# Performance work log

Measured on AMD Instinct MI355X. Metric: run time of the kernel, lower is better.

## Reference

```python
import jax, jax.numpy as jnp
import numpy as np
import math

B, L, NH, HD = 2, 2048, 8, 128
C = NH * HD            # hidden size
K = 3                  # short_conv_L
EMB, ORDER = 33, 64    # hyena filter emb_dim / order


def setup_inputs() -> dict:
    key = jax.random.key(0)
    ks = jax.random.split(key, 10)
    f32 = jnp.float32
    return {
        "query_layer": jax.random.normal(ks[0], (L, B, NH, HD), f32),
        "key_layer": jax.random.normal(ks[1], (L, B, NH, HD), f32),
        "value_layer": jax.random.normal(ks[2], (L, B, NH, HD), f32),
        # depthwise short conv params: [3(qkv), C, 1, K] / [3, C]
        "short_conv_weight": jax.random.normal(ks[3], (3, C, 1, K), f32) * 0.3,
        "short_conv_bias": jax.random.normal(ks[4], (3, C), f32) * 0.02,
        # D term of the long conv, shape [head_dim]
        "long_conv_bias": jax.random.normal(ks[5], (HD,), f32) * 0.1,
        # hyena filter MLP (torch Linear convention: W [out, in])
        "lin0_w": jax.random.normal(ks[6], (ORDER, EMB), f32) * (1.0 / np.sqrt(EMB)),
        "lin0_b": jnp.zeros((ORDER,), f32),
        "lin1_w": jax.random.normal(ks[7], (ORDER, ORDER), f32) * (1.0 / np.sqrt(ORDER)),
        "lin1_b": jnp.zeros((ORDER,), f32),
        "lin2_w": jax.random.normal(ks[8], (ORDER, ORDER), f32) * (1.0 / np.sqrt(ORDER)),
        "lin2_b": jnp.zeros((ORDER,), f32),
        "freq": jnp.ones((1, ORDER), f32),  # Sin activation freq (w=1), shared across layers
        "final_w": jax.random.normal(ks[9], (HD, ORDER), f32) * (1.0 / np.sqrt(ORDER)),
        # exponential modulation decay rates, [1,1,HD], as initialized in the module
        "mod_weight": jnp.linspace(math.log(0.01) / 1.5, math.log(0.01) / 0.3, HD,
                                   dtype=f32)[None, None],
    }


def _depthwise_conv(x, w, b):
    # x [B,C,L], w [C,1,K], b [C]; causal: pad K-1 both sides, keep first L
    y = jax.lax.conv_general_dilated(
        x, w, window_strides=(1,), padding=[(K - 1, K - 1)],
        feature_group_count=C, dimension_numbers=("NCH", "OIH", "NCH"))
    return y[..., :L] + b[None, :, None]


def _hyena_filter(lin0_w, lin0_b, lin1_w, lin1_b, lin2_w, lin2_b, freq, final_w, mod_weight):
    t = jnp.linspace(0.0, 1.0, L)[None, :, None]              # [1,L,1]
    bands = (EMB - 1) // 2
    w_ang = 2.0 * jnp.pi * jnp.linspace(0.0, L - 1.0, L) / L  # [L]
    f = jnp.linspace(1e-4, bands - 1.0, bands)                # [bands]
    theta = w_ang[:, None] * f[None, :]                       # [L,bands]; z = exp(-1j f w)
    z = jnp.concatenate([t[0], jnp.cos(theta), -jnp.sin(theta)], axis=-1)[None]  # [1,L,EMB]
    h = jnp.sin(freq * (z @ lin0_w.T + lin0_b))
    h = jnp.sin(freq * (h @ lin1_w.T + lin1_b))
    h = jnp.sin(freq * (h @ lin2_w.T + lin2_b))
    h = h @ final_w.T                                         # [1,L,HD]
    h = h * jnp.exp(-t * jnp.abs(mod_weight))                 # exponential modulation
    return h[0].T                                             # [HD, L]


def _fftconv_heads(k, kern, D, q, v):
    # mirrors fftconv_heads_ref with head_dim=NH: channels split as (h=HD, d=NH)
    b = k.shape[0]
    kr = k.reshape(b, HD, NH, L).transpose(0, 2, 1, 3)  # b nh hd L  (d1 axis)
    vr = v.reshape(b, HD, NH, L).transpose(0, 2, 1, 3)  # b nh hd L  (d2 axis)
    qr = q.reshape(b, HD, NH, L).transpose(0, 2, 1, 3)  # b nh hd L
    kv = kr[:, :, None] * vr[:, None]                   # [b, nh, nh, hd, L]
    n = 2 * L
    kv_f = jnp.fft.rfft(kv, n=n) / n
    kern_f = jnp.fft.rfft(kern, n=n)                    # [HD, n//2+1]
    y = jnp.fft.irfft(kv_f * kern_f, n=n, norm="forward")[..., :L]
    out = y + kv * D[:, None]                           # D over head_dim axis
    out = (out * qr[:, :, None]).sum(axis=1)            # _mul_sum over d1 -> [b, nh, hd, L]
    return out.transpose(0, 2, 1, 3).reshape(b, C, L)   # 'b d2 h l -> b (h d2) l'


def reference(query_layer, key_layer, value_layer, short_conv_weight, short_conv_bias,
              long_conv_bias, lin0_w, lin0_b, lin1_w, lin1_b, lin2_w, lin2_b,
              freq, final_w, mod_weight):
    # 'sq b np hn -> b (np hn) sq'
    q = jnp.transpose(query_layer, (1, 2, 3, 0)).reshape(B, C, L)
    k = jnp.transpose(key_layer, (1, 2, 3, 0)).reshape(B, C, L)
    v = jnp.transpose(value_layer, (1, 2, 3, 0)).reshape(B, C, L)
    q = _depthwise_conv(q, short_conv_weight[0], short_conv_bias[0])
    k = _depthwise_conv(k, short_conv_weight[1], short_conv_bias[1])
    v = _depthwise_conv(v, short_conv_weight[2], short_conv_bias[2])
    filt = _hyena_filter(lin0_w, lin0_b, lin1_w, lin1_b, lin2_w, lin2_b,
                         freq, final_w, mod_weight)
    # module calls fftconv_heads_ref(k=value, ..., q=query, v=key)
    y = _fftconv_heads(v, filt, long_conv_bias, q=q, v=k)
    # 'b (np hn) sq -> b np sq hn'
    return y.reshape(B, NH, HD, L).transpose(0, 1, 3, 2)
```

## Files before the change

kernel.cpp:

```cpp
#include <hip/hip_runtime.h>
#include <stdint.h>
#include <string.h>

#define L_SEQ 2048
#define B_SZ 2
#define NHH 8
#define HDD 128
#define C_SZ 1024
#define EMB_D 33
#define ORD 64
#define BANDS 16
#define FSTRIDE (L_SEQ + 256)
#define FRS_S 2568
#define FRS_FILL 2176

typedef _Float16 f16;
typedef f16 f16x8 __attribute__((ext_vector_type(8)));
typedef f16 f16x4 __attribute__((ext_vector_type(4)));
typedef float f32x4 __attribute__((ext_vector_type(4)));

__global__ void filter_kernel(const float* __restrict__ w0, const float* __restrict__ b0,
                              const float* __restrict__ w1, const float* __restrict__ b1,
                              const float* __restrict__ w2, const float* __restrict__ b2,
                              const float* __restrict__ fr, const float* __restrict__ wf,
                              const float* __restrict__ md, const float* __restrict__ Dv,
                              float* __restrict__ filt) {
  int tid = threadIdx.x;
  int o = tid & 63;
  int lq = tid >> 6;
  int l = blockIdx.x * 4 + lq;

  if (blockIdx.x < 128) filt[(size_t)blockIdx.x * FSTRIDE + tid] = 0.0f;

  __shared__ float zs[4][EMB_D];
  __shared__ float hs[4][ORD];
  __shared__ float gs[4][ORD];

  float t = (float)l / (float)(L_SEQ - 1);
  float wang = 6.2831853071795864f * (float)l / (float)L_SEQ;
  const float fstep = (15.0f - 1e-4f) / 15.0f;

  if (o == 0) zs[lq][0] = t;
  if (o >= 1 && o < 1 + BANDS) {
    int j = o - 1;
    float fj = 1e-4f + fstep * (float)j;
    zs[lq][1 + j] = cosf(wang * fj);
  }
  if (o >= 1 + BANDS && o < 1 + 2 * BANDS) {
    int j = o - 1 - BANDS;
    float fj = 1e-4f + fstep * (float)j;
    zs[lq][1 + BANDS + j] = -sinf(wang * fj);
  }
  __syncthreads();

  float fo = fr[o];
  float a = b0[o];
  for (int e = 0; e < EMB_D; ++e) a += zs[lq][e] * w0[o * EMB_D + e];
  hs[lq][o] = sinf(fo * a);
  __syncthreads();

  a = b1[o];
  for (int e = 0; e < ORD; ++e) a += hs[lq][e] * w1[o * ORD + e];
  gs[lq][o] = sinf(fo * a);
  __syncthreads();

  a = b2[o];
  for (int e = 0; e < ORD; ++e) a += gs[lq][e] * w2[o * ORD + e];
  float h3 = sinf(fo * a);
  __syncthreads();
  hs[lq][o] = h3;
  __syncthreads();

  #pragma unroll
  for (int pass = 0; pass < 2; ++pass) {
    int hd = pass * 64 + o;
    float acc = 0.0f;
    for (int e = 0; e < ORD; ++e) acc += hs[lq][e] * wf[hd * ORD + e];
    float val = acc * expf(-t * fabsf(md[hd]));
    if (l == 0) val += Dv[hd];
    filt[(size_t)hd * FSTRIDE + 256 + l] = val;
  }
}

#define TLC 64
__global__ void shortconv_kernel(const float* __restrict__ q_in,
                                 const float* __restrict__ k_in,
                                 const float* __restrict__ v_in,
                                 const float* __restrict__ scw,
                                 const float* __restrict__ scb,
                                 float* __restrict__ AqT, f16* __restrict__ Akt16,
                                 f16* __restrict__ Avt16) {
  int bid = blockIdx.x;
  int lt = bid & 31;
  int np = (bid >> 5) & 7;
  int b = bid >> 8;
  int l0 = lt * TLC;
  int tid = threadIdx.x;

  __shared__ float xs[TLC + 2][HDD + 4];
  __shared__ float wcs[HDD][4];

  const float* ins[3] = {q_in, k_in, v_in};

  for (int tsr = 0; tsr < 3; ++tsr) {
    const float* x = ins[tsr];
    if (tid < HDD) {
      int c = np * HDD + tid;
      wcs[tid][0] = scw[(tsr * C_SZ + c) * 3 + 0];
      wcs[tid][1] = scw[(tsr * C_SZ + c) * 3 + 1];
      wcs[tid][2] = scw[(tsr * C_SZ + c) * 3 + 2];
      wcs[tid][3] = scb[tsr * C_SZ + c];
    }
    for (int idx = tid; idx < (TLC + 2) * HDD; idx += 256) {
      int row = idx >> 7, hn = idx & 127;
      int l = l0 - 2 + row;
      float val = 0.0f;
      if (l >= 0) val = x[(((size_t)l * B_SZ + b) * NHH + np) * HDD + hn];
      xs[row][hn] = val;
    }
    __syncthreads();

    int n1 = tid & 7;
    int lp = tid >> 3;
    for (int hdi = 0; hdi < 16; ++hdi) {
      int hn = hdi * 8 + n1;
      float cw0 = wcs[hn][0], cw1 = wcs[hn][1], cw2 = wcs[hn][2], cb = wcs[hn][3];
      int hd = np * 16 + hdi;
      #pragma unroll
      for (int half = 0; half < 2; ++half) {
        int ll = half * 32 + lp;
        float y = cb + cw0 * xs[ll][hn] + cw1 * xs[ll + 1][hn]
                     + cw2 * xs[ll + 2][hn];
        int l = l0 + ll;
        if (tsr == 0) {
          AqT[(((size_t)b * HDD + hd) * NHH + n1) * L_SEQ + l] = y;
        } else {
          int ch = l >> 7, m = l & 127;
          int off = (n1 << 8) | ((m << 1) ^ (n1 << 4));
          char* base = (tsr == 1) ? (char*)Akt16 : (char*)Avt16;
          *(f16*)(base + ((((size_t)(b * HDD + hd)) * 16 + ch) << 11) + off) = (f16)y;
        }
      }
    }
    __syncthreads();
  }
}

__global__ void __launch_bounds__(256, 3)
hyena_main(const float* __restrict__ AqT, const f16* __restrict__ Akt16,
           const f16* __restrict__ Avt16, const float* __restrict__ filt,
           float* __restrict__ out) {
  int bid = blockIdx.x;
  int pr = bid >> 8;
  int hd = bid & 127;
  int b  = (bid >> 7) & 1;
  int tid = threadIdx.x;
  int w = tid >> 6;
  int lane = tid & 63;
  int r = lane & 15;
  int p = lane >> 4;
  int a = (15 - r) & 7;

  __shared__ f16 FRS[8][FRS_S];
  __shared__ f16 AV[3][1024];
  __shared__ f16 AK[3][1024];

  const float* frow = filt + (size_t)hd * FSTRIDE + 256;
  const char* avtg = (const char*)Avt16 + (((size_t)(b * HDD + hd)) * 16 << 11);
  const char* aktg = (const char*)Akt16 + (((size_t)(b * HDD + hd)) * 16 << 11);
  const float* aqtb = AqT + ((size_t)b * HDD + hd) * NHH * L_SEQ;
  int np = hd >> 4, hnb = (hd & 15) * 8;

  for (int aa = 0; aa < 8; ++aa) {
    for (int z4 = tid * 4; z4 < FRS_FILL; z4 += 1024) {
      const float* s = frow + (2044 - aa - z4);
      float4 v;
      __builtin_memcpy(&v, s, 16);
      f16x4 o = {(f16)v.w, (f16)v.z, (f16)v.y, (f16)v.x};
      *(f16x4*)&FRS[aa][z4] = o;
    }
  }

  f32x4 acc[2][4];

  auto dma = [&](int c, int bi) {
    const char* srcb = (w >> 1) ? aktg : avtg;
    f16* dstb = (w >> 1) ? &AK[bi][(w & 1) * 512] : &AV[bi][(w & 1) * 512];
    const char* src = srcb + ((size_t)c << 11) + (w & 1) * 1024 + lane * 16;
    __builtin_amdgcn_global_load_lds((const unsigned int*)src,
                                     (unsigned int*)dstb, 16, 0, 0);
  };

  auto unit = [&](int lt, int c, int bi) {
    int dy = 2047 - (lt - c) * 128;
    int zb = dy - r - a + p * 8 - 112 + 16 * (3 - w);
    f16x8 f[6];
    #pragma unroll
    for (int j = 0; j < 6; ++j)
      f[j] = *(const f16x8*)&FRS[a][zb + 32 * j];
    int ky = r & 7;
    __builtin_amdgcn_s_setprio(1);
    #pragma unroll
    for (int s = 0; s < 4; ++s) {
      f16x8 kf = *(const f16x8*)&AK[bi][ky * 128 + ((s * 32 + p * 8) ^ (ky * 8))];
      #pragma unroll
      for (int nt = 0; nt < 4; ++nt) {
        int vy = nt * 2 + (r >> 3);
        f16x8 vf = *(const f16x8*)&AV[bi][vy * 128 + ((s * 32 + p * 8) ^ (vy * 8))];
        f16x8 bf = vf * kf;
        acc[0][nt] = __builtin_amdgcn_mfma_f32_16x16x32_f16(
            f[s + 2], bf, acc[0][nt], 0, 0, 0);
        acc[1][nt] = __builtin_amdgcn_mfma_f32_16x16x32_f16(
            f[s], bf, acc[1][nt], 0, 0, 0);
      }
    }
    __builtin_amdgcn_s_setprio(0);
  };

  auto epilogue = [&](int lt) {
    int l0 = lt * 128;
    int hi = r >> 3;
    int n2 = r & 7;
    #pragma unroll
    for (int mi = 0; mi < 2; ++mi) {
      int mt = w + 4 * mi;
      float4 qv[4];
      #pragma unroll
      for (int nt = 0; nt < 4; ++nt)
        qv[nt] = *(const float4*)(aqtb + (size_t)(nt * 2 + hi) * L_SEQ
                                  + l0 + mt * 16 + p * 4);
      #pragma unroll
      for (int reg = 0; reg < 4; ++reg) {
        float pv = qv[0][reg] * acc[mi][0][reg] + qv[1][reg] * acc[mi][1][reg]
                 + qv[2][reg] * acc[mi][2][reg] + qv[3][reg] * acc[mi][3][reg];
        pv += __shfl_xor(pv, 8, 64);
        if (r < 8) {
          int i = mt * 16 + p * 4 + reg;
          out[(((size_t)b * NHH + np) * L_SEQ + (l0 + i)) * HDD + hnb + n2] = pv;
        }
      }
    }
  };

  auto run_pass = [&](int lt, int NC) {
    #pragma unroll
    for (int mi = 0; mi < 2; ++mi)
      #pragma unroll
      for (int nt = 0; nt < 4; ++nt)
        acc[mi][nt] = f32x4{0.f, 0.f, 0.f, 0.f};
    dma(0, 0);
    if (NC > 1) dma(1, 1);
    for (int c = 0; c < NC; ++c) {
      if (c + 1 < NC)
        asm volatile("s_waitcnt vmcnt(1) lgkmcnt(0)" ::: "memory");
      else
        asm volatile("s_waitcnt vmcnt(0) lgkmcnt(0)" ::: "memory");
      __builtin_amdgcn_s_barrier();
      __builtin_amdgcn_sched_barrier(0);
      if (c + 2 < NC) {
        int bi2 = c + 2; bi2 -= (bi2 >= 3) ? 3 : 0; bi2 -= (bi2 >= 3) ? 3 : 0;
        dma(c + 2, (c + 2) % 3);
      }
      unit(lt, c, c % 3);
    }
    epilogue(lt);
    __syncthreads();
  };

  run_pass(pr, pr + 1);
  run_pass(15 - pr, 16 - pr);
}

extern "C" void kernel_launch(void* const* d_in, const int* in_sizes, int n_in,
                              void* d_out, int out_size, void* d_ws, size_t ws_size,
                              hipStream_t stream) {
  const float* q_in = (const float*)d_in[0];
  const float* k_in = (const float*)d_in[1];
  const float* v_in = (const float*)d_in[2];
  const float* scw  = (const float*)d_in[3];
  const float* scb  = (const float*)d_in[4];
  const float* Dv   = (const float*)d_in[5];
  const float* w0   = (const float*)d_in[6];
  const float* b0   = (const float*)d_in[7];
  const float* w1   = (const float*)d_in[8];
  const float* b1   = (const float*)d_in[9];
  const float* w2   = (const float*)d_in[10];
  const float* b2   = (const float*)d_in[11];
  const float* fr   = (const float*)d_in[12];
  const float* wf   = (const float*)d_in[13];
  const float* md   = (const float*)d_in[14];

  float* ws   = (float*)d_ws;
  float* filt = ws;
  float* AqT  = ws + (size_t)HDD * FSTRIDE;
  f16*   Akt16 = (f16*)(AqT + (size_t)B_SZ * HDD * L_SEQ * NHH);
  f16*   Avt16 = Akt16 + (size_t)B_SZ * HDD * 16 * 1024;

  filter_kernel<<<512, 256, 0, stream>>>(w0, b0, w1, b1, w2, b2, fr, wf, md, Dv, filt);
  shortconv_kernel<<<512, 256, 0, stream>>>(q_in, k_in, v_in, scw, scb, AqT, Akt16, Avt16);
  hyena_main<<<2048, 256, 0, stream>>>(AqT, Akt16, Avt16, filt, (float*)d_out);
}
```

Measured before the change: 148.4 us.

## Fuse the two output-tile passes to share loaded key/value chunks

The two sequential passes over output tiles (low and high) are merged into one loop over chunks. Each loaded K/V chunk and its elementwise product now feed both accumulator sets, so the low tile's chunks are not loaded twice. The pipeline moves to a 4-deep buffer processed two chunks per barrier, and the filter LDS row stride is shrunk to offset the larger buffers. The cost is doubled accumulator registers, which may reduce occupancy under the 3-blocks launch bound, and a branchy per-chunk do_lo path.

```diff
diff --git a/kernel.cpp b/kernel.cpp
--- a/kernel.cpp
+++ b/kernel.cpp
@@ -11,7 +11,7 @@
 #define ORD 64
 #define BANDS 16
 #define FSTRIDE (L_SEQ + 256)
-#define FRS_S 2568
+#define FRS_S 2184
 #define FRS_FILL 2176
 
 typedef _Float16 f16;
@@ -161,9 +161,13 @@
   int p = lane >> 4;
   int a = (15 - r) & 7;
 
+  const int LT_hi = 15 - pr;
+  const int LT_lo = pr;
+  const int NCc = 16 - pr;
+
   __shared__ f16 FRS[8][FRS_S];
-  __shared__ f16 AV[3][1024];
-  __shared__ f16 AK[3][1024];
+  __shared__ f16 AV[4][1024];
+  __shared__ f16 AK[4][1024];
 
   const float* frow = filt + (size_t)hd * FSTRIDE + 256;
   const char* avtg = (const char*)Avt16 + (((size_t)(b * HDD + hd)) * 16 << 11);
@@ -181,7 +185,14 @@
     }
   }
 
-  f32x4 acc[2][4];
+  f32x4 aH[2][4], aL[2][4];
+  #pragma unroll
+  for (int mi = 0; mi < 2; ++mi)
+    #pragma unroll
+    for (int nt = 0; nt < 4; ++nt) {
+      aH[mi][nt] = f32x4{0.f, 0.f, 0.f, 0.f};
+      aL[mi][nt] = f32x4{0.f, 0.f, 0.f, 0.f};
+    }
 
   auto dma = [&](int c, int bi) {
     const char* srcb = (w >> 1) ? aktg : avtg;
@@ -191,13 +202,21 @@
                                      (unsigned int*)dstb, 16, 0, 0);
   };
 
-  auto unit = [&](int lt, int c, int bi) {
-    int dy = 2047 - (lt - c) * 128;
-    int zb = dy - r - a + p * 8 - 112 + 16 * (3 - w);
-    f16x8 f[6];
+  auto chunk_body = [&](int c) {
+    int bi = c & 3;
+    bool do_lo = (c <= LT_lo);
+    int zcom = p * 8 - 112 + 16 * (3 - w) - r - a;
+    int zbH = 2047 - (LT_hi - c) * 128 + zcom;
+    f16x8 fH[6], fL[6];
     #pragma unroll
     for (int j = 0; j < 6; ++j)
-      f[j] = *(const f16x8*)&FRS[a][zb + 32 * j];
+      fH[j] = *(const f16x8*)&FRS[a][zbH + 32 * j];
+    if (do_lo) {
+      int zbL = 2047 - (LT_lo - c) * 128 + zcom;
+      #pragma unroll
+      for (int j = 0; j < 6; ++j)
+        fL[j] = *(const f16x8*)&FRS[a][zbL + 32 * j];
+    }
     int ky = r & 7;
     __builtin_amdgcn_s_setprio(1);
     #pragma unroll
@@ -208,16 +227,22 @@
         int vy = nt * 2 + (r >> 3);
         f16x8 vf = *(const f16x8*)&AV[bi][vy * 128 + ((s * 32 + p * 8) ^ (vy * 8))];
         f16x8 bf = vf * kf;
-        acc[0][nt] = __builtin_amdgcn_mfma_f32_16x16x32_f16(
-            f[s + 2], bf, acc[0][nt], 0, 0, 0);
-        acc[1][nt] = __builtin_amdgcn_mfma_f32_16x16x32_f16(
-            f[s], bf, acc[1][nt], 0, 0, 0);
+        aH[0][nt] = __builtin_amdgcn_mfma_f32_16x16x32_f16(
+            fH[s + 2], bf, aH[0][nt], 0, 0, 0);
+        aH[1][nt] = __builtin_amdgcn_mfma_f32_16x16x32_f16(
+            fH[s], bf, aH[1][nt], 0, 0, 0);
+        if (do_lo) {
+          aL[0][nt] = __builtin_amdgcn_mfma_f32_16x16x32_f16(
+              fL[s + 2], bf, aL[0][nt], 0, 0, 0);
+          aL[1][nt] = __builtin_amdgcn_mfma_f32_16x16x32_f16(
+              fL[s], bf, aL[1][nt], 0, 0, 0);
+        }
       }
     }
     __builtin_amdgcn_s_setprio(0);
   };
 
-  auto epilogue = [&](int lt) {
+  auto epilogue = [&](int lt, f32x4 (&acc)[2][4]) {
     int l0 = lt * 128;
     int hi = r >> 3;
     int n2 = r & 7;
@@ -242,33 +267,22 @@
     }
   };
 
-  auto run_pass = [&](int lt, int NC) {
-    #pragma unroll
-    for (int mi = 0; mi < 2; ++mi)
-      #pragma unroll
-      for (int nt = 0; nt < 4; ++nt)
-        acc[mi][nt] = f32x4{0.f, 0.f, 0.f, 0.f};
-    dma(0, 0);
-    if (NC > 1) dma(1, 1);
-    for (int c = 0; c < NC; ++c) {
-      if (c + 1 < NC)
-        asm volatile("s_waitcnt vmcnt(1) lgkmcnt(0)" ::: "memory");
-      else
-        asm volatile("s_waitcnt vmcnt(0) lgkmcnt(0)" ::: "memory");
-      __builtin_amdgcn_s_barrier();
-      __builtin_amdgcn_sched_barrier(0);
-      if (c + 2 < NC) {
-        int bi2 = c + 2; bi2 -= (bi2 >= 3) ? 3 : 0; bi2 -= (bi2 >= 3) ? 3 : 0;
-        dma(c + 2, (c + 2) % 3);
-      }
-      unit(lt, c, c % 3);
-    }
-    epilogue(lt);
-    __syncthreads();
-  };
-
-  run_pass(pr, pr + 1);
-  run_pass(15 - pr, 16 - pr);
+  dma(0, 0); dma(1, 1);
+
+  int iters = (NCc + 1) >> 1;
+  for (int it = 0; it < iters; ++it) {
+    int c0 = 2 * it, c1 = 2 * it + 1;
+    asm volatile("s_waitcnt vmcnt(0) lgkmcnt(0)" ::: "memory");
+    __builtin_amdgcn_s_barrier();
+    __builtin_amdgcn_sched_barrier(0);
+    if (c0 + 2 < NCc) dma(c0 + 2, (c0 + 2) & 3);
+    if (c1 + 2 < NCc) dma(c1 + 2, (c1 + 2) & 3);
+    chunk_body(c0);
+    if (c1 < NCc) chunk_body(c1);
+  }
+
+  epilogue(LT_hi, aH);
+  epilogue(LT_lo, aL);
 }
 
 extern "C" void kernel_launch(void* const* d_in, const int* in_sizes, int n_in,
```

New measurement: 146.6 us. About the same (-1.2%).
